# Performance work log

Measured on AMD Instinct MI355X. Metric: run time of the kernel, lower is better.

## Reference

```python
import jax, jax.numpy as jnp
import numpy as np

SCALE = 88.0        # img_scale used to normalize pixel coords (== feature width)
GRID_H = 4.0        # grid_height
GRID_RES_Y = 0.5    # grid_res[2]


def setup_inputs() -> dict:
    rng = np.random.RandomState(0)
    B, N, C, H, W = 2, 6, 64, 32, 88
    Dg = 128  # BEV grid cells per side
    features = rng.randn(B, N, C, H, W).astype(np.float32)
    # intrinsics at feature resolution
    fx, fy, cx, cy = 40.0, 40.0, 44.0, 16.0
    k = np.array([[fx, 0, cx], [0, fy, cy], [0, 0, 1]], np.float32)
    ks = np.broadcast_to(k, (B, N, 3, 3)).copy()
    # extrinsics: 6 cameras with yaw spaced 60 deg, small translation
    imu2cs = np.zeros((B, N, 3, 4), np.float32)
    for n in range(N):
        th = 2.0 * np.pi * n / N
        R = np.array([[np.cos(th), 0, np.sin(th)],
                      [0, 1, 0],
                      [-np.sin(th), 0, np.cos(th)]], np.float32)
        imu2cs[:, n, :, :3] = R
        imu2cs[:, n, :, 3] = np.array([0.123, 1.4, 0.234], np.float32)
    post_rots = np.broadcast_to(np.eye(3, dtype=np.float32), (B, N, 3, 3)).copy()
    post_trans = np.zeros((B, N, 3), np.float32)
    post_trans[..., :2] = 0.5
    # distortion coeffs (small) + fisheye/pinhole flag in last slot
    undists = ((rng.rand(B, N, 7).astype(np.float32) - 0.5) * 0.02)
    undists[..., 6] = np.broadcast_to((np.arange(N) % 2).astype(np.float32), (B, N))
    # BEV grid corners: (B, Dg+1, Dg+1, 3) with coords (x, 0, z)
    xs = np.linspace(-40.0, 40.0, Dg + 1).astype(np.float32)
    zs = (np.linspace(-40.0, 40.0, Dg + 1) + 0.017).astype(np.float32)
    gx, gz = np.meshgrid(xs, zs, indexing='xy')  # [d, w] = (xs[w], zs[d])
    g = np.stack([gx, np.zeros_like(gx), gz], axis=-1)
    grid = np.broadcast_to(g, (B, Dg + 1, Dg + 1, 3)).copy()
    return {
        'features': jnp.asarray(features), 'ks': jnp.asarray(ks),
        'imu2cs': jnp.asarray(imu2cs), 'post_rots': jnp.asarray(post_rots),
        'post_trans': jnp.asarray(post_trans), 'undists': jnp.asarray(undists),
        'grid': jnp.asarray(grid), 'drop_idx': 6,  # 6 == no camera dropped
    }


def _forward(features, ks, imu2cs, post_rots, post_trans, undists, grid):
    B, N, C, H, W = features.shape
    # y_corners[:-1] -> (Hc, 3) offsets (0, y, 0)
    y = -jnp.arange(0.0, GRID_H, GRID_RES_Y) + GRID_H / 2.0
    Hc = y.shape[0] - 1
    y_off = jnp.stack([jnp.zeros(Hc), y[:-1], jnp.zeros(Hc)], axis=-1)
    corners = grid[:, None, :-1, :-1, :] + y_off[None, :, None, None, :]  # (B,Hc,D,Wg,3)
    D_, Wg = corners.shape[2], corners.shape[3]
    calib = jnp.einsum('bnij,bnjk->bnik', ks, imu2cs)  # (B,N,3,4)
    # perspective projection
    hom = jnp.einsum('bnij,bhdwj->bnhdwi', calib[..., :3], corners) \
        + calib[..., 3][:, :, None, None, None, :]      # (B,N,Hc,D,Wg,3)
    m = (hom[..., 2] > 0).astype(features.dtype)[..., None]  # z>0 mask
    hom = hom * jnp.concatenate([m, m, jnp.ones_like(m)], axis=-1)
    pts = hom[..., :2] / hom[..., 2:3]                   # (B,N,Hc,D,Wg,2)
    # distortion (fisheye or pinhole per camera, selected by undists[...,-1])
    fx = ks[..., 0, 0][:, :, None, None, None]
    fy = ks[..., 1, 1][:, :, None, None, None]
    cx = ks[..., 0, 2][:, :, None, None, None]
    cy = ks[..., 1, 2][:, :, None, None, None]
    x = (pts[..., 0] - cx) / fx
    yv = (pts[..., 1] - cy) / fy
    d = [undists[..., i][:, :, None, None, None] for i in range(7)]
    # fisheye: theta polynomial (coeffs D0,D1,D2,D5)
    r = jnp.sqrt(x * x + yv * yv)
    th = jnp.arctan(r)
    t2 = th * th
    rad = th * (1 + d[0] * t2 + d[1] * t2 ** 2 + d[2] * t2 ** 3 + d[5] * t2 ** 4) / r
    fish = jnp.stack([x * rad * fx + cx, yv * rad * fy + cy], axis=-1)
    # pinhole: radial k1,k2,k3 + tangential p1,p2
    r2 = x * x + yv * yv
    radial = 1 + d[0] * r2 + d[1] * r2 * r2 + d[2] * r2 * r2 * r2
    xp = x * radial + 2 * d[3] * x * yv + d[4] * (r2 + 2 * x * x)
    yp = yv * radial + d[3] * (r2 + 2 * yv * yv) + 2 * d[4] * x * yv
    pin = jnp.stack([xp * fx + cx, yp * fy + cy], axis=-1)
    is_fish = (undists[..., 6] == 1)[:, :, None, None, None, None]
    dist = jnp.where(is_fish, fish, pin) * m             # flag[...,:-1] masking
    # post-augmentation transform
    pts2 = jnp.einsum('bnij,bnhdwj->bnhdwi', post_rots[:, :, :2, :2], dist) \
         + post_trans[:, :, None, None, None, :2]
    norm = jnp.clip(2.0 * pts2 / SCALE - 1.0, -1.0, 1.0)
    P = Hc * D_ * Wg
    coords = norm.reshape(B, N, P, 2)
    visible = ((coords[..., 0] > -1) & (coords[..., 0] < 1) &
               (coords[..., 1] > -1) & (coords[..., 1] < 1))
    # bilinear grid_sample, align_corners=True, padding_mode='border'
    gx = (coords[..., 0] + 1.0) * 0.5 * (W - 1)
    gy = (coords[..., 1] + 1.0) * 0.5 * (H - 1)
    x0 = jnp.floor(gx)
    y0 = jnp.floor(gy)
    wx = gx - x0
    wy = gy - y0
    x0i = jnp.clip(x0, 0, W - 1).astype(jnp.int32)
    x1i = jnp.clip(x0 + 1, 0, W - 1).astype(jnp.int32)
    y0i = jnp.clip(y0, 0, H - 1).astype(jnp.int32)
    y1i = jnp.clip(y0 + 1, 0, H - 1).astype(jnp.int32)
    fflat = features.reshape(B, N, C, H * W)
    def gat(yi, xi):
        return jnp.take_along_axis(fflat, (yi * W + xi)[:, :, None, :], axis=3)
    w00 = ((1 - wx) * (1 - wy))[:, :, None, :]
    w01 = (wx * (1 - wy))[:, :, None, :]
    w10 = ((1 - wx) * wy)[:, :, None, :]
    w11 = (wx * wy)[:, :, None, :]
    vox = (gat(y0i, x0i) * w00 + gat(y0i, x1i) * w01 +
           gat(y1i, x0i) * w10 + gat(y1i, x1i) * w11)    # (B,N,C,P)
    vox = vox * visible[:, :, None, :].astype(vox.dtype)
    vox = vox.reshape(B, N, C * Hc, D_, Wg)              # neck='2d'
    return jnp.max(vox, axis=1)                          # max over cameras


def reference(features, ks, imu2cs, post_rots, post_trans, undists, grid, drop_idx):
    # drop_idx == num_cams means no camera is dropped (original skips i in drop_idx)
    return _forward(features, ks, imu2cs, post_rots, post_trans, undists, grid)
```

## Files before the change

kernel.cpp:

```cpp
#include <hip/hip_runtime.h>
#include <math.h>

typedef _Float16 h2 __attribute__((ext_vector_type(2)));

#define BB 2
#define NN 6
#define CC 64
#define HH 32
#define WW 88
#define HC 7
#define DG 128
#define HWP (HH*WW)
#define GSTR 129
#define OUTCH (CC*HC)
#define CSTRIDE (HC*DG*DG)

__global__ __launch_bounds__(256) void transpose_feat_f16_kernel(
    const float* __restrict__ f, _Float16* __restrict__ ft) {
  __shared__ float lds[64 * 65];
  int blk = blockIdx.x;
  int bn = blk / 44;
  int pxbase = (blk % 44) * 64;
  int tid = threadIdx.x;
  #pragma unroll
  for (int i = 0; i < 16; ++i) {
    int idx = i * 256 + tid;
    int ch = idx >> 6, px = idx & 63;
    lds[px * 65 + ch] = f[((size_t)bn * CC + ch) * HWP + pxbase + px];
  }
  __syncthreads();
  int px = tid >> 2, cg = (tid & 3) * 16;
  union { h2 hv[8]; int4 v4[2]; } u;
  #pragma unroll
  for (int k = 0; k < 8; ++k) {
    float lo = lds[px * 65 + cg + 2 * k];
    float hi = lds[px * 65 + cg + 2 * k + 1];
    u.hv[k] = (h2){(_Float16)lo, (_Float16)hi};
  }
  int4* dst = (int4*)(ft + ((size_t)bn * HWP + pxbase + px) * CC + cg);
  dst[0] = u.v4[0];
  dst[1] = u.v4[1];
}

template<bool TRANS>
__global__ __launch_bounds__(256) void oft_main_kernel(
    const float* __restrict__ feats,
    const _Float16* __restrict__ featT,
    const float* __restrict__ ks, const float* __restrict__ imu,
    const float* __restrict__ prots, const float* __restrict__ ptrans,
    const float* __restrict__ und, const float* __restrict__ grid,
    float* __restrict__ out) {
  __shared__ float s_par[NN * 32];
  __shared__ __align__(16) h2 s_beh2[NN * 32];

  int blk = blockIdx.x;
  int cs  = blk & 1;
  int rr  = blk >> 1;
  int b  = rr / (HC * 64);
  int r  = rr % (HC * 64);
  int hc = r / 64;
  int d  = (r % 64) * 2 + threadIdx.y;
  int w  = threadIdx.x;
  int tid = threadIdx.y * 128 + threadIdx.x;
  int chbase = cs * 32;

  if (tid < NN) {
    int n = tid;
    int cam = b * NN + n;
    const float* K = ks + cam * 9;
    const float* M = imu + cam * 12;
    float* P = &s_par[n * 32];
    #pragma unroll
    for (int i = 0; i < 3; ++i)
      #pragma unroll
      for (int k = 0; k < 4; ++k)
        P[i * 4 + k] = K[i*3+0]*M[0*4+k] + K[i*3+1]*M[1*4+k] + K[i*3+2]*M[2*4+k];
    P[12] = K[0]; P[13] = K[4]; P[14] = K[2]; P[15] = K[5];
    const float* u = und + cam * 7;
    #pragma unroll
    for (int i = 0; i < 6; ++i) P[16 + i] = u[i];
    P[23] = u[6];
    const float* R = prots + cam * 9;
    P[24] = R[0]; P[25] = R[1]; P[26] = R[3]; P[27] = R[4];
    const float* T = ptrans + cam * 3;
    P[28] = T[0]; P[29] = T[1];
    float nx = fminf(fmaxf(2.0f * T[0] / 88.0f - 1.0f, -1.f), 1.f);
    float ny = fminf(fmaxf(2.0f * T[1] / 88.0f - 1.0f, -1.f), 1.f);
    bool vis = (nx > -1.f) && (nx < 1.f) && (ny > -1.f) && (ny < 1.f);
    P[30] = vis ? 1.f : 0.f;
    P[31] = 0.f;
  }
  __syncthreads();

  if (tid < NN * 32) {
    int n = tid >> 5, m = tid & 31;
    const float* P = &s_par[n * 32];
    float v0 = 0.f, v1 = 0.f;
    if (P[30] != 0.f) {
      float nx = fminf(fmaxf(2.0f * P[28] / 88.0f - 1.0f, -1.f), 1.f);
      float ny = fminf(fmaxf(2.0f * P[29] / 88.0f - 1.0f, -1.f), 1.f);
      float gx = (nx + 1.f) * 0.5f * (float)(WW - 1);
      float gy = (ny + 1.f) * 0.5f * (float)(HH - 1);
      float x0f = floorf(gx), y0f = floorf(gy);
      float wx = gx - x0f, wy = gy - y0f;
      int x0 = (int)fminf(fmaxf(x0f,        0.f), (float)(WW - 1));
      int x1 = (int)fminf(fmaxf(x0f + 1.f,  0.f), (float)(WW - 1));
      int y0 = (int)fminf(fmaxf(y0f,        0.f), (float)(HH - 1));
      int y1 = (int)fminf(fmaxf(y0f + 1.f,  0.f), (float)(HH - 1));
      float w00 = (1.f - wx) * (1.f - wy), w01 = wx * (1.f - wy);
      float w10 = (1.f - wx) * wy,         w11 = wx * wy;
      const float* fb0 = feats + ((size_t)(b * NN + n) * CC + 2*m) * HWP;
      const float* fb1 = fb0 + HWP;
      v0 = fb0[y0*WW+x0]*w00 + fb0[y0*WW+x1]*w01 + fb0[y1*WW+x0]*w10 + fb0[y1*WW+x1]*w11;
      v1 = fb1[y0*WW+x0]*w00 + fb1[y0*WW+x1]*w01 + fb1[y1*WW+x0]*w10 + fb1[y1*WW+x1]*w11;
    }
    s_beh2[tid] = (h2){(_Float16)v0, (_Float16)v1};
  }
  __syncthreads();

  size_t gidx = (((size_t)b * GSTR + d) * GSTR + w) * 3;
  float px = grid[gidx];
  float py = grid[gidx + 1] + (2.0f - 0.5f * (float)hc);
  float pz = grid[gidx + 2];

  int   mode[NN];
  int   off[NN];
  float fwx[NN], fwy[NN];
  bool any0 = false;
  #pragma unroll
  for (int n = 0; n < NN; ++n) {
    const float* P = &s_par[n * 32];
    float hz = P[8]*px + P[9]*py + P[10]*pz + P[11];
    int md = 0;
    if (hz > 0.f) {
      float hx = P[0]*px + P[1]*py + P[2]*pz + P[3];
      float hy = P[4]*px + P[5]*py + P[6]*pz + P[7];
      float ptx = hx / hz, pty = hy / hz;
      float fx = P[12], fy = P[13], cx = P[14], cy = P[15];
      float xn = (ptx - cx) / fx, yn = (pty - cy) / fy;
      float dx, dy;
      if (P[23] == 1.0f) {
        float r2 = xn*xn + yn*yn;
        float rr2 = sqrtf(r2);
        float th = atanf(rr2);
        float t2 = th*th, t4 = t2*t2;
        float poly = 1.f + P[16]*t2 + P[17]*t4 + P[18]*(t4*t2) + P[21]*(t4*t4);
        float rad = th * poly / rr2;
        dx = xn * rad * fx + cx;
        dy = yn * rad * fy + cy;
      } else {
        float r2 = xn*xn + yn*yn;
        float radial = 1.f + P[16]*r2 + P[17]*r2*r2 + P[18]*r2*r2*r2;
        float xp = xn*radial + 2.f*P[19]*xn*yn + P[20]*(r2 + 2.f*xn*xn);
        float yp = yn*radial + P[19]*(r2 + 2.f*yn*yn) + 2.f*P[20]*xn*yn;
        dx = xp * fx + cx;
        dy = yp * fy + cy;
      }
      float p2x = P[24]*dx + P[25]*dy + P[28];
      float p2y = P[26]*dx + P[27]*dy + P[29];
      float nx = fminf(fmaxf(2.0f * p2x / 88.0f - 1.0f, -1.f), 1.f);
      float ny = fminf(fmaxf(2.0f * p2y / 88.0f - 1.0f, -1.f), 1.f);
      bool visible = (nx > -1.f) && (nx < 1.f) && (ny > -1.f) && (ny < 1.f);
      if (visible) {
        float gx = (nx + 1.f) * 0.5f * (float)(WW - 1);
        float gy = (ny + 1.f) * 0.5f * (float)(HH - 1);
        float x0f = floorf(gx), y0f = floorf(gy);
        fwx[n] = gx - x0f;
        fwy[n] = gy - y0f;
        int x0 = (int)fminf(fmaxf(x0f, 0.f), (float)(WW - 1));
        int y0 = (int)fminf(fmaxf(y0f, 0.f), (float)(HH - 1));
        off[n] = y0 * WW + x0;
        md = 1;
      } else {
        any0 = true;
      }
    } else {
      if (P[30] != 0.f) md = 2; else any0 = true;
    }
    mode[n] = md;
  }

  h2 acc2[16];
  _Float16 iv = any0 ? (_Float16)0.f : (_Float16)(-INFINITY);
  h2 inith = (h2){iv, iv};
  #pragma unroll
  for (int m = 0; m < 16; ++m) acc2[m] = inith;

  #pragma unroll
  for (int n = 0; n < NN; ++n) {
    if (mode[n] == 1) {
      float wxv = fwx[n], wyv = fwy[n];
      _Float16 hw00 = (_Float16)((1.f - wxv) * (1.f - wyv));
      _Float16 hw01 = (_Float16)(wxv * (1.f - wyv));
      _Float16 hw10 = (_Float16)((1.f - wxv) * wyv);
      _Float16 hw11 = (_Float16)(wxv * wyv);
      h2 w00h = (h2){hw00, hw00}, w01h = (h2){hw01, hw01};
      h2 w10h = (h2){hw10, hw10}, w11h = (h2){hw11, hw11};
      if (TRANS) {
        const int4* t00 = (const int4*)(featT +
            ((size_t)(b*NN+n)*HWP + off[n]) * CC + chbase);
        const int4* t01 = t00 + (CC/8);
        const int4* t10 = t00 + (size_t)WW*(CC/8);
        const int4* t11 = t10 + (CC/8);
        #pragma unroll
        for (int j = 0; j < 4; ++j) {
          int4 A = t00[j], B4 = t01[j], C4 = t10[j], D4 = t11[j];
          const h2* av = (const h2*)&A;
          const h2* bv = (const h2*)&B4;
          const h2* cv = (const h2*)&C4;
          const h2* dv = (const h2*)&D4;
          #pragma unroll
          for (int k = 0; k < 4; ++k) {
            h2 v = av[k]*w00h + bv[k]*w01h + cv[k]*w10h + dv[k]*w11h;
            acc2[j*4+k] = __builtin_elementwise_max(acc2[j*4+k], v);
          }
        }
      } else {
        float w00 = (1.f - wxv) * (1.f - wyv), w01 = wxv * (1.f - wyv);
        float w10 = (1.f - wxv) * wyv,         w11 = wxv * wyv;
        const float* fb = feats + ((size_t)(b*NN+n) * CC + chbase) * HWP + off[n];
        #pragma unroll
        for (int m = 0; m < 16; ++m) {
          const float* p0 = fb + (size_t)(2*m) * HWP;
          const float* p1 = p0 + HWP;
          float v0 = p0[0]*w00 + p0[1]*w01 + p0[WW]*w10 + p0[WW+1]*w11;
          float v1 = p1[0]*w00 + p1[1]*w01 + p1[WW]*w10 + p1[WW+1]*w11;
          acc2[m] = __builtin_elementwise_max(acc2[m],
                        (h2){(_Float16)v0, (_Float16)v1});
        }
      }
    } else if (mode[n] == 2) {
      const h2* bp = &s_beh2[n * 32 + cs * 16];
      #pragma unroll
      for (int m = 0; m < 16; ++m)
        acc2[m] = __builtin_elementwise_max(acc2[m], bp[m]);
    }
  }

  float* op = out + (((size_t)b * OUTCH + hc) * DG + d) * DG + w
            + (size_t)chbase * CSTRIDE;
  #pragma unroll
  for (int m = 0; m < 16; ++m) {
    op[(size_t)(2*m)   * CSTRIDE] = (float)acc2[m].x;
    op[(size_t)(2*m+1) * CSTRIDE] = (float)acc2[m].y;
  }
}

extern "C" void kernel_launch(void* const* d_in, const int* in_sizes, int n_in,
                              void* d_out, int out_size, void* d_ws, size_t ws_size,
                              hipStream_t stream) {
  const float* feats  = (const float*)d_in[0];
  const float* ks     = (const float*)d_in[1];
  const float* imu    = (const float*)d_in[2];
  const float* prots  = (const float*)d_in[3];
  const float* ptrans = (const float*)d_in[4];
  const float* und    = (const float*)d_in[5];
  const float* grid   = (const float*)d_in[6];
  float* out = (float*)d_out;

  size_t featT_bytes = (size_t)BB * NN * HWP * CC * sizeof(_Float16);
  bool trans = (d_ws != nullptr) && (ws_size >= featT_bytes);
  _Float16* featT = (_Float16*)d_ws;

  dim3 mblock(128, 2);
  dim3 mgrid(BB * HC * 64 * 2);

  if (trans) {
    transpose_feat_f16_kernel<<<BB * NN * 44, 256, 0, stream>>>(feats, featT);
    oft_main_kernel<true><<<mgrid, mblock, 0, stream>>>(
        feats, featT, ks, imu, prots, ptrans, und, grid, out);
  } else {
    oft_main_kernel<false><<<mgrid, mblock, 0, stream>>>(
        feats, featT, ks, imu, prots, ptrans, und, grid, out);
  }
}
```

Before: 126.2 us.

## Split per-camera setup into its own kernel and remap gather to lanes-per-channel

Camera parameter and behind-camera value setup moves into a separate single-block kernel that writes to workspace. Per-block recomputation of that work goes away. The main gather kernel now covers 16 BEV columns per block with 512 threads: 96 threads project points and store the results in shared memory, then each lane gathers one channel pair, so neighbouring lanes read contiguous half-precision channel data. Results are transposed through shared memory for float2 output stores, which adds an extra kernel launch, more synchronisation and a narrower per-thread load width.

Result: slower. 132.7 us (+5.1%).

```diff
diff --git a/kernel.cpp b/kernel.cpp
--- a/kernel.cpp
+++ b/kernel.cpp
@@ -42,34 +42,18 @@
   dst[1] = u.v4[1];
 }
 
-template<bool TRANS>
-__global__ __launch_bounds__(256) void oft_main_kernel(
-    const float* __restrict__ feats,
-    const _Float16* __restrict__ featT,
-    const float* __restrict__ ks, const float* __restrict__ imu,
-    const float* __restrict__ prots, const float* __restrict__ ptrans,
-    const float* __restrict__ und, const float* __restrict__ grid,
-    float* __restrict__ out) {
-  __shared__ float s_par[NN * 32];
-  __shared__ __align__(16) h2 s_beh2[NN * 32];
-
-  int blk = blockIdx.x;
-  int cs  = blk & 1;
-  int rr  = blk >> 1;
-  int b  = rr / (HC * 64);
-  int r  = rr % (HC * 64);
-  int hc = r / 64;
-  int d  = (r % 64) * 2 + threadIdx.y;
-  int w  = threadIdx.x;
-  int tid = threadIdx.y * 128 + threadIdx.x;
-  int chbase = cs * 32;
-
-  if (tid < NN) {
-    int n = tid;
-    int cam = b * NN + n;
+__global__ __launch_bounds__(384) void setup_kernel(
+    const float* __restrict__ feats, const float* __restrict__ ks,
+    const float* __restrict__ imu, const float* __restrict__ prots,
+    const float* __restrict__ ptrans, const float* __restrict__ und,
+    float* __restrict__ wsPar, h2* __restrict__ wsBeh) {
+  __shared__ float lds_par[BB * NN * 32];
+  int t = threadIdx.x;
+  if (t < BB * NN) {
+    int cam = t;
     const float* K = ks + cam * 9;
     const float* M = imu + cam * 12;
-    float* P = &s_par[n * 32];
+    float* P = &lds_par[cam * 32];
     #pragma unroll
     for (int i = 0; i < 3; ++i)
       #pragma unroll
@@ -89,49 +73,74 @@
     bool vis = (nx > -1.f) && (nx < 1.f) && (ny > -1.f) && (ny < 1.f);
     P[30] = vis ? 1.f : 0.f;
     P[31] = 0.f;
-  }
-  __syncthreads();
+    #pragma unroll
+    for (int i = 0; i < 32; ++i) wsPar[cam * 32 + i] = P[i];
+  }
+  __syncthreads();
+  int cam = t >> 5, m = t & 31;
+  const float* P = &lds_par[cam * 32];
+  float v0 = 0.f, v1 = 0.f;
+  if (P[30] != 0.f) {
+    float nx = fminf(fmaxf(2.0f * P[28] / 88.0f - 1.0f, -1.f), 1.f);
+    float ny = fminf(fmaxf(2.0f * P[29] / 88.0f - 1.0f, -1.f), 1.f);
+    float gx = (nx + 1.f) * 0.5f * (float)(WW - 1);
+    float gy = (ny + 1.f) * 0.5f * (float)(HH - 1);
+    float x0f = floorf(gx), y0f = floorf(gy);
+    float wx = gx - x0f, wy = gy - y0f;
+    int x0 = (int)fminf(fmaxf(x0f,       0.f), (float)(WW - 1));
+    int x1 = (int)fminf(fmaxf(x0f + 1.f, 0.f), (float)(WW - 1));
+    int y0 = (int)fminf(fmaxf(y0f,       0.f), (float)(HH - 1));
+    int y1 = (int)fminf(fmaxf(y0f + 1.f, 0.f), (float)(HH - 1));
+    float w00 = (1.f - wx) * (1.f - wy), w01 = wx * (1.f - wy);
+    float w10 = (1.f - wx) * wy,         w11 = wx * wy;
+    const float* fb0 = feats + ((size_t)cam * CC + 2*m) * HWP;
+    const float* fb1 = fb0 + HWP;
+    v0 = fb0[y0*WW+x0]*w00 + fb0[y0*WW+x1]*w01 + fb0[y1*WW+x0]*w10 + fb0[y1*WW+x1]*w11;
+    v1 = fb1[y0*WW+x0]*w00 + fb1[y0*WW+x1]*w01 + fb1[y1*WW+x0]*w10 + fb1[y1*WW+x1]*w11;
+  }
+  wsBeh[cam * 32 + m] = (h2){(_Float16)v0, (_Float16)v1};
+}
+
+__global__ __launch_bounds__(512) void oft_gather_kernel(
+    const _Float16* __restrict__ featT,
+    const float* __restrict__ wsPar,
+    const h2* __restrict__ wsBeh,
+    const float* __restrict__ grid,
+    float* __restrict__ out) {
+  __shared__ float s_parf[NN * 32];
+  __shared__ h2    s_beh [NN * 32];
+  __shared__ int   s_mode[NN * 16];
+  __shared__ int   s_off [NN * 16];
+  __shared__ float s_wx  [NN * 16];
+  __shared__ float s_wy  [NN * 16];
+  __shared__ h2    s_acc [16 * 33];
+
+  int blk = blockIdx.x;
+  int wt = blk & 7;  int rest = blk >> 3;
+  int d  = rest & 127; rest >>= 7;
+  int hc = rest % 7;
+  int b  = rest / 7;
+  int w0 = wt * 16;
+  int tid = threadIdx.x;
 
   if (tid < NN * 32) {
-    int n = tid >> 5, m = tid & 31;
-    const float* P = &s_par[n * 32];
-    float v0 = 0.f, v1 = 0.f;
-    if (P[30] != 0.f) {
-      float nx = fminf(fmaxf(2.0f * P[28] / 88.0f - 1.0f, -1.f), 1.f);
-      float ny = fminf(fmaxf(2.0f * P[29] / 88.0f - 1.0f, -1.f), 1.f);
-      float gx = (nx + 1.f) * 0.5f * (float)(WW - 1);
-      float gy = (ny + 1.f) * 0.5f * (float)(HH - 1);
-      float x0f = floorf(gx), y0f = floorf(gy);
-      float wx = gx - x0f, wy = gy - y0f;
-      int x0 = (int)fminf(fmaxf(x0f,        0.f), (float)(WW - 1));
-      int x1 = (int)fminf(fmaxf(x0f + 1.f,  0.f), (float)(WW - 1));
-      int y0 = (int)fminf(fmaxf(y0f,        0.f), (float)(HH - 1));
-      int y1 = (int)fminf(fmaxf(y0f + 1.f,  0.f), (float)(HH - 1));
-      float w00 = (1.f - wx) * (1.f - wy), w01 = wx * (1.f - wy);
-      float w10 = (1.f - wx) * wy,         w11 = wx * wy;
-      const float* fb0 = feats + ((size_t)(b * NN + n) * CC + 2*m) * HWP;
-      const float* fb1 = fb0 + HWP;
-      v0 = fb0[y0*WW+x0]*w00 + fb0[y0*WW+x1]*w01 + fb0[y1*WW+x0]*w10 + fb0[y1*WW+x1]*w11;
-      v1 = fb1[y0*WW+x0]*w00 + fb1[y0*WW+x1]*w01 + fb1[y1*WW+x0]*w10 + fb1[y1*WW+x1]*w11;
-    }
-    s_beh2[tid] = (h2){(_Float16)v0, (_Float16)v1};
-  }
-  __syncthreads();
-
-  size_t gidx = (((size_t)b * GSTR + d) * GSTR + w) * 3;
-  float px = grid[gidx];
-  float py = grid[gidx + 1] + (2.0f - 0.5f * (float)hc);
-  float pz = grid[gidx + 2];
-
-  int   mode[NN];
-  int   off[NN];
-  float fwx[NN], fwy[NN];
-  bool any0 = false;
-  #pragma unroll
-  for (int n = 0; n < NN; ++n) {
-    const float* P = &s_par[n * 32];
+    s_parf[tid] = wsPar[(size_t)(b * NN) * 32 + tid];
+    s_beh[tid]  = wsBeh[(size_t)(b * NN) * 32 + tid];
+  }
+  __syncthreads();
+
+  if (tid < 96) {
+    int p = tid & 15, n = tid >> 4;
+    const float* P = &s_parf[n * 32];
+    int w = w0 + p;
+    size_t gidx = (((size_t)b * GSTR + d) * GSTR + w) * 3;
+    float px = grid[gidx];
+    float py = grid[gidx + 1] + (2.0f - 0.5f * (float)hc);
+    float pz = grid[gidx + 2];
+
+    int md = 0, offv = 0;
+    float fwx = 0.f, fwy = 0.f;
     float hz = P[8]*px + P[9]*py + P[10]*pz + P[11];
-    int md = 0;
     if (hz > 0.f) {
       float hx = P[0]*px + P[1]*py + P[2]*pz + P[3];
       float hy = P[4]*px + P[5]*py + P[6]*pz + P[7];
@@ -165,69 +174,219 @@
         float gx = (nx + 1.f) * 0.5f * (float)(WW - 1);
         float gy = (ny + 1.f) * 0.5f * (float)(HH - 1);
         float x0f = floorf(gx), y0f = floorf(gy);
+        fwx = gx - x0f;
+        fwy = gy - y0f;
+        int x0 = (int)fminf(fmaxf(x0f, 0.f), (float)(WW - 1));
+        int y0 = (int)fminf(fmaxf(y0f, 0.f), (float)(HH - 1));
+        offv = y0 * WW + x0;
+        md = 1;
+      }
+    } else {
+      if (P[30] != 0.f) md = 2;
+    }
+    s_mode[n*16+p] = md;
+    s_off [n*16+p] = offv;
+    s_wx  [n*16+p] = fwx;
+    s_wy  [n*16+p] = fwy;
+  }
+  __syncthreads();
+
+  int lane = tid & 63;
+  int p = (tid >> 6) * 2 + (lane >> 5);
+  int m = lane & 31;
+
+  bool a0 = false;
+  #pragma unroll
+  for (int n = 0; n < NN; ++n) a0 |= (s_mode[n*16+p] == 0);
+  _Float16 iv = a0 ? (_Float16)0.f : (_Float16)(-INFINITY);
+  h2 acc = (h2){iv, iv};
+
+  const _Float16* fbase = featT + (size_t)(b * NN) * HWP * CC + 2 * m;
+  #pragma unroll
+  for (int n = 0; n < NN; ++n) {
+    int md = s_mode[n*16+p];
+    if (md == 1) {
+      int offv = s_off[n*16+p];
+      float wxv = s_wx[n*16+p], wyv = s_wy[n*16+p];
+      const _Float16* rec = fbase + ((size_t)n * HWP + offv) * CC;
+      h2 aq = *(const h2*)(rec);
+      h2 bq = *(const h2*)(rec + CC);
+      h2 cq = *(const h2*)(rec + WW*CC);
+      h2 dq = *(const h2*)(rec + WW*CC + CC);
+      _Float16 h00 = (_Float16)((1.f - wxv) * (1.f - wyv));
+      _Float16 h01 = (_Float16)(wxv * (1.f - wyv));
+      _Float16 h10 = (_Float16)((1.f - wxv) * wyv);
+      _Float16 h11 = (_Float16)(wxv * wyv);
+      h2 v = aq * (h2){h00,h00} + bq * (h2){h01,h01}
+           + cq * (h2){h10,h10} + dq * (h2){h11,h11};
+      acc = __builtin_elementwise_max(acc, v);
+    } else if (md == 2) {
+      acc = __builtin_elementwise_max(acc, s_beh[n*32 + m]);
+    }
+  }
+  s_acc[p * 33 + m] = acc;
+  __syncthreads();
+
+  int c = tid >> 3, ws8 = tid & 7;
+  h2 v0 = s_acc[(ws8*2)   * 33 + (c >> 1)];
+  h2 v1 = s_acc[(ws8*2+1) * 33 + (c >> 1)];
+  int comp = c & 1;
+  float2 o;
+  o.x = (float)(comp ? v0.y : v0.x);
+  o.y = (float)(comp ? v1.y : v1.x);
+  float* op = out + (((size_t)b * OUTCH + c * HC + hc) * DG + d) * DG + w0 + ws8 * 2;
+  *(float2*)op = o;
+}
+
+__global__ __launch_bounds__(256) void oft_fallback_kernel(
+    const float* __restrict__ feats,
+    const float* __restrict__ ks, const float* __restrict__ imu,
+    const float* __restrict__ prots, const float* __restrict__ ptrans,
+    const float* __restrict__ und, const float* __restrict__ grid,
+    float* __restrict__ out) {
+  __shared__ float s_par[NN * 32];
+  __shared__ __align__(16) h2 s_beh2[NN * 32];
+  int blk = blockIdx.x;
+  int cs  = blk & 1;
+  int rr  = blk >> 1;
+  int b  = rr / (HC * 64);
+  int r  = rr % (HC * 64);
+  int hc = r / 64;
+  int d  = (r % 64) * 2 + threadIdx.y;
+  int w  = threadIdx.x;
+  int tid = threadIdx.y * 128 + threadIdx.x;
+  int chbase = cs * 32;
+  if (tid < NN) {
+    int n = tid;
+    int cam = b * NN + n;
+    const float* K = ks + cam * 9;
+    const float* M = imu + cam * 12;
+    float* P = &s_par[n * 32];
+    #pragma unroll
+    for (int i = 0; i < 3; ++i)
+      #pragma unroll
+      for (int k = 0; k < 4; ++k)
+        P[i * 4 + k] = K[i*3+0]*M[0*4+k] + K[i*3+1]*M[1*4+k] + K[i*3+2]*M[2*4+k];
+    P[12] = K[0]; P[13] = K[4]; P[14] = K[2]; P[15] = K[5];
+    const float* u = und + cam * 7;
+    #pragma unroll
+    for (int i = 0; i < 6; ++i) P[16 + i] = u[i];
+    P[23] = u[6];
+    const float* R = prots + cam * 9;
+    P[24] = R[0]; P[25] = R[1]; P[26] = R[3]; P[27] = R[4];
+    const float* T = ptrans + cam * 3;
+    P[28] = T[0]; P[29] = T[1];
+    float nx = fminf(fmaxf(2.0f * T[0] / 88.0f - 1.0f, -1.f), 1.f);
+    float ny = fminf(fmaxf(2.0f * T[1] / 88.0f - 1.0f, -1.f), 1.f);
+    bool vis = (nx > -1.f) && (nx < 1.f) && (ny > -1.f) && (ny < 1.f);
+    P[30] = vis ? 1.f : 0.f;
+    P[31] = 0.f;
+  }
+  __syncthreads();
+  if (tid < NN * 32) {
+    int n = tid >> 5, m = tid & 31;
+    const float* P = &s_par[n * 32];
+    float v0 = 0.f, v1 = 0.f;
+    if (P[30] != 0.f) {
+      float nx = fminf(fmaxf(2.0f * P[28] / 88.0f - 1.0f, -1.f), 1.f);
+      float ny = fminf(fmaxf(2.0f * P[29] / 88.0f - 1.0f, -1.f), 1.f);
+      float gx = (nx + 1.f) * 0.5f * (float)(WW - 1);
+      float gy = (ny + 1.f) * 0.5f * (float)(HH - 1);
+      float x0f = floorf(gx), y0f = floorf(gy);
+      float wx = gx - x0f, wy = gy - y0f;
+      int x0 = (int)fminf(fmaxf(x0f,       0.f), (float)(WW - 1));
+      int x1 = (int)fminf(fmaxf(x0f + 1.f, 0.f), (float)(WW - 1));
+      int y0 = (int)fminf(fmaxf(y0f,       0.f), (float)(HH - 1));
+      int y1 = (int)fminf(fmaxf(y0f + 1.f, 0.f), (float)(HH - 1));
+      float w00 = (1.f - wx) * (1.f - wy), w01 = wx * (1.f - wy);
+      float w10 = (1.f - wx) * wy,         w11 = wx * wy;
+      const float* fb0 = feats + ((size_t)(b * NN + n) * CC + 2*m) * HWP;
+      const float* fb1 = fb0 + HWP;
+      v0 = fb0[y0*WW+x0]*w00 + fb0[y0*WW+x1]*w01 + fb0[y1*WW+x0]*w10 + fb0[y1*WW+x1]*w11;
+      v1 = fb1[y0*WW+x0]*w00 + fb1[y0*WW+x1]*w01 + fb1[y1*WW+x0]*w10 + fb1[y1*WW+x1]*w11;
+    }
+    s_beh2[tid] = (h2){(_Float16)v0, (_Float16)v1};
+  }
+  __syncthreads();
+  size_t gidx = (((size_t)b * GSTR + d) * GSTR + w) * 3;
+  float px = grid[gidx];
+  float py = grid[gidx + 1] + (2.0f - 0.5f * (float)hc);
+  float pz = grid[gidx + 2];
+  int   mode[NN];
+  int   off[NN];
+  float fwx[NN], fwy[NN];
+  bool any0 = false;
+  #pragma unroll
+  for (int n = 0; n < NN; ++n) {
+    const float* P = &s_par[n * 32];
+    float hz = P[8]*px + P[9]*py + P[10]*pz + P[11];
+    int md = 0;
+    if (hz > 0.f) {
+      float hx = P[0]*px + P[1]*py + P[2]*pz + P[3];
+      float hy = P[4]*px + P[5]*py + P[6]*pz + P[7];
+      float ptx = hx / hz, pty = hy / hz;
+      float fx = P[12], fy = P[13], cx = P[14], cy = P[15];
+      float xn = (ptx - cx) / fx, yn = (pty - cy) / fy;
+      float dx, dy;
+      if (P[23] == 1.0f) {
+        float r2 = xn*xn + yn*yn;
+        float rr2 = sqrtf(r2);
+        float th = atanf(rr2);
+        float t2 = th*th, t4 = t2*t2;
+        float poly = 1.f + P[16]*t2 + P[17]*t4 + P[18]*(t4*t2) + P[21]*(t4*t4);
+        float rad = th * poly / rr2;
+        dx = xn * rad * fx + cx;
+        dy = yn * rad * fy + cy;
+      } else {
+        float r2 = xn*xn + yn*yn;
+        float radial = 1.f + P[16]*r2 + P[17]*r2*r2 + P[18]*r2*r2*r2;
+        float xp = xn*radial + 2.f*P[19]*xn*yn + P[20]*(r2 + 2.f*xn*xn);
+        float yp = yn*radial + P[19]*(r2 + 2.f*yn*yn) + 2.f*P[20]*xn*yn;
+        dx = xp * fx + cx;
+        dy = yp * fy + cy;
+      }
+      float p2x = P[24]*dx + P[25]*dy + P[28];
+      float p2y = P[26]*dx + P[25 + 1]*dy + P[29];
+      p2y = P[26]*dx + P[27]*dy + P[29];
+      float nx = fminf(fmaxf(2.0f * p2x / 88.0f - 1.0f, -1.f), 1.f);
+      float ny = fminf(fmaxf(2.0f * p2y / 88.0f - 1.0f, -1.f), 1.f);
+      bool visible = (nx > -1.f) && (nx < 1.f) && (ny > -1.f) && (ny < 1.f);
+      if (visible) {
+        float gx = (nx + 1.f) * 0.5f * (float)(WW - 1);
+        float gy = (ny + 1.f) * 0.5f * (float)(HH - 1);
+        float x0f = floorf(gx), y0f = floorf(gy);
         fwx[n] = gx - x0f;
         fwy[n] = gy - y0f;
         int x0 = (int)fminf(fmaxf(x0f, 0.f), (float)(WW - 1));
         int y0 = (int)fminf(fmaxf(y0f, 0.f), (float)(HH - 1));
         off[n] = y0 * WW + x0;
         md = 1;
-      } else {
-        any0 = true;
-      }
+      } else any0 = true;
     } else {
       if (P[30] != 0.f) md = 2; else any0 = true;
     }
     mode[n] = md;
   }
-
   h2 acc2[16];
   _Float16 iv = any0 ? (_Float16)0.f : (_Float16)(-INFINITY);
   h2 inith = (h2){iv, iv};
   #pragma unroll
   for (int m = 0; m < 16; ++m) acc2[m] = inith;
-
   #pragma unroll
   for (int n = 0; n < NN; ++n) {
     if (mode[n] == 1) {
       float wxv = fwx[n], wyv = fwy[n];
-      _Float16 hw00 = (_Float16)((1.f - wxv) * (1.f - wyv));
-      _Float16 hw01 = (_Float16)(wxv * (1.f - wyv));
-      _Float16 hw10 = (_Float16)((1.f - wxv) * wyv);
-      _Float16 hw11 = (_Float16)(wxv * wyv);
-      h2 w00h = (h2){hw00, hw00}, w01h = (h2){hw01, hw01};
-      h2 w10h = (h2){hw10, hw10}, w11h = (h2){hw11, hw11};
-      if (TRANS) {
-        const int4* t00 = (const int4*)(featT +
-            ((size_t)(b*NN+n)*HWP + off[n]) * CC + chbase);
-        const int4* t01 = t00 + (CC/8);
-        const int4* t10 = t00 + (size_t)WW*(CC/8);
-        const int4* t11 = t10 + (CC/8);
-        #pragma unroll
-        for (int j = 0; j < 4; ++j) {
-          int4 A = t00[j], B4 = t01[j], C4 = t10[j], D4 = t11[j];
-          const h2* av = (const h2*)&A;
-          const h2* bv = (const h2*)&B4;
-          const h2* cv = (const h2*)&C4;
-          const h2* dv = (const h2*)&D4;
-          #pragma unroll
-          for (int k = 0; k < 4; ++k) {
-            h2 v = av[k]*w00h + bv[k]*w01h + cv[k]*w10h + dv[k]*w11h;
-            acc2[j*4+k] = __builtin_elementwise_max(acc2[j*4+k], v);
-          }
-        }
-      } else {
-        float w00 = (1.f - wxv) * (1.f - wyv), w01 = wxv * (1.f - wyv);
-        float w10 = (1.f - wxv) * wyv,         w11 = wxv * wyv;
-        const float* fb = feats + ((size_t)(b*NN+n) * CC + chbase) * HWP + off[n];
-        #pragma unroll
-        for (int m = 0; m < 16; ++m) {
-          const float* p0 = fb + (size_t)(2*m) * HWP;
-          const float* p1 = p0 + HWP;
-          float v0 = p0[0]*w00 + p0[1]*w01 + p0[WW]*w10 + p0[WW+1]*w11;
-          float v1 = p1[0]*w00 + p1[1]*w01 + p1[WW]*w10 + p1[WW+1]*w11;
-          acc2[m] = __builtin_elementwise_max(acc2[m],
-                        (h2){(_Float16)v0, (_Float16)v1});
-        }
+      float w00 = (1.f - wxv) * (1.f - wyv), w01 = wxv * (1.f - wyv);
+      float w10 = (1.f - wxv) * wyv,         w11 = wxv * wyv;
+      const float* fb = feats + ((size_t)(b*NN+n) * CC + chbase) * HWP + off[n];
+      #pragma unroll
+      for (int m = 0; m < 16; ++m) {
+        const float* p0 = fb + (size_t)(2*m) * HWP;
+        const float* p1 = p0 + HWP;
+        float v0 = p0[0]*w00 + p0[1]*w01 + p0[WW]*w10 + p0[WW+1]*w11;
+        float v1 = p1[0]*w00 + p1[1]*w01 + p1[WW]*w10 + p1[WW+1]*w11;
+        acc2[m] = __builtin_elementwise_max(acc2[m],
+                      (h2){(_Float16)v0, (_Float16)v1});
       }
     } else if (mode[n] == 2) {
       const h2* bp = &s_beh2[n * 32 + cs * 16];
@@ -236,7 +395,6 @@
         acc2[m] = __builtin_elementwise_max(acc2[m], bp[m]);
     }
   }
-
   float* op = out + (((size_t)b * OUTCH + hc) * DG + d) * DG + w
             + (size_t)chbase * CSTRIDE;
   #pragma unroll
@@ -259,18 +417,24 @@
   float* out = (float*)d_out;
 
   size_t featT_bytes = (size_t)BB * NN * HWP * CC * sizeof(_Float16);
-  bool trans = (d_ws != nullptr) && (ws_size >= featT_bytes);
-  _Float16* featT = (_Float16*)d_ws;
-
-  dim3 mblock(128, 2);
-  dim3 mgrid(BB * HC * 64 * 2);
+  size_t par_bytes   = (size_t)BB * NN * 32 * sizeof(float);
+  size_t beh_bytes   = (size_t)BB * NN * 32 * sizeof(h2);
+  size_t need = featT_bytes + par_bytes + beh_bytes;
+  bool trans = (d_ws != nullptr) && (ws_size >= need);
 
   if (trans) {
+    _Float16* featT = (_Float16*)d_ws;
+    float* wsPar = (float*)((char*)d_ws + featT_bytes);
+    h2* wsBeh = (h2*)((char*)d_ws + featT_bytes + par_bytes);
     transpose_feat_f16_kernel<<<BB * NN * 44, 256, 0, stream>>>(feats, featT);
-    oft_main_kernel<true><<<mgrid, mblock, 0, stream>>>(
-        feats, featT, ks, imu, prots, ptrans, und, grid, out);
+    setup_kernel<<<1, 384, 0, stream>>>(feats, ks, imu, prots, ptrans, und,
+                                        wsPar, wsBeh);
+    oft_gather_kernel<<<BB * HC * DG * (DG/16), 512, 0, stream>>>(
+        featT, wsPar, wsBeh, grid, out);
   } else {
-    oft_main_kernel<false><<<mgrid, mblock, 0, stream>>>(
-        feats, featT, ks, imu, prots, ptrans, und, grid, out);
+    dim3 mblock(128, 2);
+    dim3 mgrid(BB * HC * 64 * 2);
+    oft_fallback_kernel<<<mgrid, mblock, 0, stream>>>(
+        feats, ks, imu, prots, ptrans, und, grid, out);
   }
 }
```
